# Performance work log

Hardware: AMD Instinct MI355X
Metric: run time of the kernel (lower is better)

## Reference

```python
import jax, jax.numpy as jnp
import numpy as np
from jax import lax

KH = KW = 3
DIL = 4
D = DIL * (KH - 1) + 1  # dilated (effective) kernel extent = 9
PAD = 4
STRIDE = 1


def setup_inputs() -> dict:
    key = jax.random.key(0)
    k1, k2, k3, k4 = jax.random.split(key, 4)
    Cin, Cout, B, H, W = 128, 128, 16, 112, 112
    fan_in = Cin * KH * KW
    x = jax.random.normal(k1, (B, Cin, H, W), dtype=jnp.float32)
    weight = jax.random.normal(k2, (Cout, Cin, KH, KW), dtype=jnp.float32) / np.sqrt(fan_in)
    # learnable positions: offsets of each kernel point inside the dilated kernel
    P = jax.random.normal(k3, (2, Cout, Cin, KH, KW), dtype=jnp.float32) * (DIL / 2.0)
    bias = jax.random.normal(k4, (Cout,), dtype=jnp.float32) * 0.01
    return {"x": x, "weight": weight, "P": P, "bias": bias}


def _construct_kernel(weight, P):
    # Place each kernel point at its (learnable) continuous position inside the
    # D x D dilated kernel via bilinear interpolation (DCLS construction).
    O, C, kh, kw = weight.shape
    base_h = jnp.arange(kh, dtype=weight.dtype) * DIL  # regular dilated grid
    base_w = jnp.arange(kw, dtype=weight.dtype) * DIL
    p_h = jnp.clip(base_h[None, None, :, None] + P[0], 0.0, D - 1)  # (O,C,kh,kw)
    p_w = jnp.clip(base_w[None, None, None, :] + P[1], 0.0, D - 1)
    fh = jnp.floor(p_h)
    fw = jnp.floor(p_w)
    rh = p_h - fh  # fractional residuals -> bilinear weights
    rw = p_w - fw
    ih = fh.astype(jnp.int32)
    iw = fw.astype(jnp.int32)
    ih1 = jnp.minimum(ih + 1, D - 1)
    iw1 = jnp.minimum(iw + 1, D - 1)
    o = jnp.arange(O)[:, None, None, None]
    c = jnp.arange(C)[None, :, None, None]
    K = jnp.zeros((O, C, D, D), dtype=weight.dtype)
    K = K.at[o, c, ih, iw].add(weight * (1 - rh) * (1 - rw))
    K = K.at[o, c, ih1, iw].add(weight * rh * (1 - rw))
    K = K.at[o, c, ih, iw1].add(weight * (1 - rh) * rw)
    K = K.at[o, c, ih1, iw1].add(weight * rh * rw)
    return K


def reference(x, weight, P, bias):
    K = _construct_kernel(weight, P)  # (Cout, Cin, D, D)
    out = lax.conv_general_dilated(
        x, K,
        window_strides=(STRIDE, STRIDE),
        padding=[(PAD, PAD), (PAD, PAD)],
        dimension_numbers=("NCHW", "OIHW", "NCHW"),
        feature_group_count=1,
    )
    return out + bias[None, :, None, None]
```

## Files before the change

kernel.cpp:

```cpp
#include <hip/hip_runtime.h>
#include <hip/hip_bf16.h>
#include <stdint.h>


typedef __attribute__((ext_vector_type(8))) short short8;
typedef __attribute__((ext_vector_type(16))) float f32x16;

__device__ inline unsigned short f2bf(float f) {
    union { float f; unsigned int u; } v; v.f = f;
    unsigned int u = v.u;
    return (unsigned short)((u + 0x7FFFu + ((u >> 16) & 1u)) >> 16);
}

__global__ void build_K(const float* __restrict__ weight,
                        const float* __restrict__ P,
                        unsigned short* __restrict__ Kws) {
    __shared__ float sacc[128 * 81];
    int tid = threadIdx.x;
    int pair = blockIdx.x * 128 + tid;
    int o = pair >> 7, c = pair & 127;
    float* a = &sacc[tid * 81];
    for (int i = 0; i < 81; ++i) a[i] = 0.0f;
    int base = pair * 9;
    #pragma unroll
    for (int kh = 0; kh < 3; ++kh) {
        #pragma unroll
        for (int kw = 0; kw < 3; ++kw) {
            int kk = kh * 3 + kw;
            float w  = weight[base + kk];
            float p0 = P[base + kk];
            float p1 = P[128 * 128 * 9 + base + kk];
            float ph = fminf(fmaxf((float)(kh * 4) + p0, 0.0f), 8.0f);
            float pw = fminf(fmaxf((float)(kw * 4) + p1, 0.0f), 8.0f);
            float fh = floorf(ph), fw = floorf(pw);
            float rh = ph - fh, rw = pw - fw;
            int ih = (int)fh, iw = (int)fw;
            int ih1 = min(ih + 1, 8), iw1 = min(iw + 1, 8);
            a[ih  * 9 + iw ] += w * (1.0f - rh) * (1.0f - rw);
            a[ih1 * 9 + iw ] += w * rh * (1.0f - rw);
            a[ih  * 9 + iw1] += w * (1.0f - rh) * rw;
            a[ih1 * 9 + iw1] += w * rh * rw;
        }
    }
    int chunk = c >> 4, half = (c >> 3) & 1, clo = c & 7;
    for (int tap = 0; tap < 81; ++tap) {
        int idx = ((tap * 8 + chunk) * 2 + half) * 1024 + o * 8 + clo;
        Kws[idx] = f2bf(a[tap]);
    }
}

__global__ __launch_bounds__(256, 2)
void dcls_conv(const float* __restrict__ x,
               const unsigned short* __restrict__ Kws,
               const float* __restrict__ bias,
               float* __restrict__ out) {
    __shared__ __align__(16) char smem[18432 + 36864];
    char* sX = smem;
    char* sK = smem + 18432;

    int bid = blockIdx.x;
    int b   = bid / 49;
    int rem = bid % 49;
    int ty  = rem / 7, tx = rem % 7;
    int y0  = ty * 16, x0 = tx * 16;

    int tid  = threadIdx.x;
    int lane = tid & 63;
    int wave = tid >> 6;
    int mgrp = wave >> 1;
    int ngrp = wave & 1;
    int half = lane >> 5;
    int l31  = lane & 31;
    int lrow = (lane >> 4) & 1;
    int lcol = lane & 15;

    f32x16 acc[2][4];
    #pragma unroll
    for (int i = 0; i < 2; ++i)
        #pragma unroll
        for (int j = 0; j < 4; ++j)
            #pragma unroll
            for (int k = 0; k < 16; ++k) acc[i][j][k] = 0.0f;

    int preA[2];
    #pragma unroll
    for (int i = 0; i < 2; ++i)
        preA[i] = half * 2048 + ((mgrp * 2 + i) * 32 + l31) * 16;
    int preB[4];
    #pragma unroll
    for (int j = 0; j < 4; ++j)
        preB[j] = (2 * (ngrp * 4 + j) + lrow) * 768 + half * 384 + lcol * 16;

    for (int cc = 0; cc < 8; ++cc) {
        __syncthreads();
        {
            int cbase = cc * 16;
            #pragma unroll
            for (int it = 0; it < 5; ++it) {
                int u = tid + it * 256;
                if (u < 1152) {
                    int r  = u / 48;
                    int rr = u % 48;
                    int hf = rr / 24;
                    int co = rr % 24;
                    int h = y0 - 4 + r;
                    int w = x0 - 4 + co;
                    bool ok = (h >= 0) & (h < 112) & (w >= 0) & (w < 112);
                    const float* xp = x + (((b * 128 + cbase + hf * 8) * 112 + h) * 112 + w);
                    short8 v;
                    #pragma unroll
                    for (int j = 0; j < 8; ++j) {
                        float f = ok ? xp[j * 112 * 112] : 0.0f;
                        v[j] = (short)f2bf(f);
                    }
                    *(short8*)(sX + u * 16) = v;
                }
            }
        }
        for (int tg = 0; tg < 9; ++tg) {
            __syncthreads();
            #pragma unroll
            for (int t = 0; t < 9; ++t) {
                int tap = tg * 9 + t;
                const short8* src = (const short8*)(Kws + (tap * 8 + cc) * 2048);
                *(short8*)(sK + t * 4096 + tid * 16) = src[tid];
            }
            __syncthreads();
            #pragma unroll
            for (int t = 0; t < 9; ++t) {
                short8 af[2];
                #pragma unroll
                for (int i = 0; i < 2; ++i)
                    af[i] = *(const short8*)(sK + t * 4096 + preA[i]);
                short8 bfr[4];
                int tapoff = tg * 768 + t * 16;
                #pragma unroll
                for (int j = 0; j < 4; ++j)
                    bfr[j] = *(const short8*)(sX + preB[j] + tapoff);
                #pragma unroll
                for (int i = 0; i < 2; ++i)
                    #pragma unroll
                    for (int j = 0; j < 4; ++j)
                        acc[i][j] = __builtin_amdgcn_mfma_f32_32x32x16_bf16(
                            af[i], bfr[j], acc[i][j], 0, 0, 0);
            }
        }
    }

    #pragma unroll
    for (int i = 0; i < 2; ++i) {
        int ob = (mgrp * 2 + i) * 32;
        #pragma unroll
        for (int r = 0; r < 16; ++r) {
            int o = ob + (r & 3) + 8 * (r >> 2) + 4 * half;
            float bv = bias[o];
            #pragma unroll
            for (int j = 0; j < 4; ++j) {
                int nt  = ngrp * 4 + j;
                int row = y0 + 2 * nt + lrow;
                int col = x0 + lcol;
                out[((b * 128 + o) * 112 + row) * 112 + col] = acc[i][j][r] + bv;
            }
        }
    }
}

extern "C" void kernel_launch(void* const* d_in, const int* in_sizes, int n_in,
                              void* d_out, int out_size, void* d_ws, size_t ws_size,
                              hipStream_t stream) {
    const float* x      = (const float*)d_in[0];
    const float* weight = (const float*)d_in[1];
    const float* P      = (const float*)d_in[2];
    const float* bias   = (const float*)d_in[3];
    float* out = (float*)d_out;
    unsigned short* Kws = (unsigned short*)d_ws;

    build_K<<<128, 128, 0, stream>>>(weight, P, Kws);
    dcls_conv<<<784, 256, 0, stream>>>(x, Kws, bias, out);
}
```

Baseline: 619.6 us.

## Read weight fragments directly from global memory and vectorize kernel-construction stores

```diff
diff --git a/kernel.cpp b/kernel.cpp
--- a/kernel.cpp
+++ b/kernel.cpp
@@ -17,11 +17,11 @@
                         unsigned short* __restrict__ Kws) {
     __shared__ float sacc[128 * 81];
     int tid = threadIdx.x;
-    int pair = blockIdx.x * 128 + tid;
-    int o = pair >> 7, c = pair & 127;
-    float* a = &sacc[tid * 81];
+    int o = blockIdx.x;
+    int c = tid;
+    float* a = &sacc[c * 81];
     for (int i = 0; i < 81; ++i) a[i] = 0.0f;
-    int base = pair * 9;
+    int base = (o * 128 + c) * 9;
     #pragma unroll
     for (int kh = 0; kh < 3; ++kh) {
         #pragma unroll
@@ -42,10 +42,17 @@
             a[ih1 * 9 + iw1] += w * rh * rw;
         }
     }
-    int chunk = c >> 4, half = (c >> 3) & 1, clo = c & 7;
-    for (int tap = 0; tap < 81; ++tap) {
-        int idx = ((tap * 8 + chunk) * 2 + half) * 1024 + o * 8 + clo;
-        Kws[idx] = f2bf(a[tap]);
+    __syncthreads();
+    for (int u = tid; u < 1296; u += 128) {
+        int tap = u >> 4;
+        int rem = u & 15;
+        int chunk = rem >> 1, half = rem & 1;
+        int c0 = chunk * 16 + half * 8;
+        short8 v;
+        #pragma unroll
+        for (int j = 0; j < 8; ++j)
+            v[j] = (short)f2bf(sacc[(c0 + j) * 81 + tap]);
+        *(short8*)(Kws + ((tap * 8 + chunk) * 2 + half) * 1024 + o * 8) = v;
     }
 }
 
@@ -54,9 +61,7 @@
                const unsigned short* __restrict__ Kws,
                const float* __restrict__ bias,
                float* __restrict__ out) {
-    __shared__ __align__(16) char smem[18432 + 36864];
-    char* sX = smem;
-    char* sK = smem + 18432;
+    __shared__ __align__(16) char sX[18432];
 
     int bid = blockIdx.x;
     int b   = bid / 49;
@@ -82,14 +87,16 @@
             #pragma unroll
             for (int k = 0; k < 16; ++k) acc[i][j][k] = 0.0f;
 
-    int preA[2];
+    int preAu[2];
     #pragma unroll
     for (int i = 0; i < 2; ++i)
-        preA[i] = half * 2048 + ((mgrp * 2 + i) * 32 + l31) * 16;
+        preAu[i] = half * 128 + ((mgrp * 2 + i) * 32 + l31);
     int preB[4];
     #pragma unroll
     for (int j = 0; j < 4; ++j)
         preB[j] = (2 * (ngrp * 4 + j) + lrow) * 768 + half * 384 + lcol * 16;
+
+    const char* Kb = (const char*)Kws;
 
     for (int cc = 0; cc < 8; ++cc) {
         __syncthreads();
@@ -117,21 +124,17 @@
                 }
             }
         }
+        __syncthreads();
         for (int tg = 0; tg < 9; ++tg) {
-            __syncthreads();
             #pragma unroll
             for (int t = 0; t < 9; ++t) {
                 int tap = tg * 9 + t;
-                const short8* src = (const short8*)(Kws + (tap * 8 + cc) * 2048);
-                *(short8*)(sK + t * 4096 + tid * 16) = src[tid];
-            }
-            __syncthreads();
-            #pragma unroll
-            for (int t = 0; t < 9; ++t) {
+                const short8* kp =
+                    (const short8*)(Kb + ((size_t)(tap * 8 + cc) << 12));
                 short8 af[2];
                 #pragma unroll
                 for (int i = 0; i < 2; ++i)
-                    af[i] = *(const short8*)(sK + t * 4096 + preA[i]);
+                    af[i] = kp[preAu[i]];
                 short8 bfr[4];
                 int tapoff = tg * 768 + t * 16;
                 #pragma unroll
```

New measurement: 706.0 us. +13.9%, slower.
